# Performance work log

Measured on AMD Instinct MI355X. Metric: run time of the kernel, lower is better.

Reference implementation:

```python
import jax, jax.numpy as jnp
import numpy as np

N_CLASS = 20          # foreground classes (VOC)
SCORE_THR = 0.05
NMS_THR = 0.3
IMG_H, IMG_W = 600, 800
R = 2000              # number of proposed ROIs


def setup_inputs() -> dict:
    key = jax.random.key(0)
    k1, k2, k3, k4, k5 = jax.random.split(key, 5)
    # well-formed proposal boxes (y1, x1, y2, x2)
    cy = jax.random.uniform(k1, (R,), minval=0.0, maxval=float(IMG_H))
    cx = jax.random.uniform(k2, (R,), minval=0.0, maxval=float(IMG_W))
    hw = jax.random.uniform(k3, (R, 2), minval=20.0, maxval=200.0)
    h, w = hw[:, 0], hw[:, 1]
    boxes = jnp.stack([
        jnp.clip(cy - 0.5 * h, 0.0, IMG_H),
        jnp.clip(cx - 0.5 * w, 0.0, IMG_W),
        jnp.clip(cy + 0.5 * h, 0.0, IMG_H),
        jnp.clip(cx + 0.5 * w, 0.0, IMG_W),
    ], axis=1).astype(jnp.float32)
    loc = (0.2 * jax.random.normal(k4, (R, 4 * (N_CLASS + 1)))).astype(jnp.float32)
    score = (2.0 * jax.random.normal(k5, (R, N_CLASS + 1))).astype(jnp.float32)
    return {
        "proposed_roi_bboxes": boxes,
        "predicted_roi_loc": loc,
        "predicted_roi_score": score,
        "img_height": IMG_H,
        "img_width": IMG_W,
    }


def _pairwise_iou(b):
    # b: [N, 4] in (y1, x1, y2, x2); IoU is invariant to axis order
    tl = jnp.maximum(b[:, None, :2], b[None, :, :2])
    br = jnp.minimum(b[:, None, 2:], b[None, :, 2:])
    wh = jnp.clip(br - tl, 0.0)
    inter = wh[..., 0] * wh[..., 1]
    area = (b[:, 2] - b[:, 0]) * (b[:, 3] - b[:, 1])
    union = area[:, None] + area[None, :] - inter
    return inter / jnp.maximum(union, 1e-9)


def _nms_keep(boxes_sorted, valid_sorted, thr):
    # boxes sorted by descending score; returns keep mask [N]
    N = boxes_sorted.shape[0]
    iou = _pairwise_iou(boxes_sorted)          # [N, N]
    idx = jnp.arange(N)
    def body(suppressed, i):
        keep_i = valid_sorted[i] & (~suppressed[i])
        suppressed = suppressed | (keep_i & (iou[i] > thr) & (idx > i))
        return suppressed, keep_i
    _, keep = jax.lax.scan(body, jnp.zeros((N,), bool), idx)
    return keep


def _detect(proposed_roi_bboxes, predicted_roi_loc, predicted_roi_score, H, W):
    Rn = proposed_roi_bboxes.shape[0]
    C1 = N_CLASS + 1
    b = proposed_roi_bboxes
    loc = predicted_roi_loc.reshape(Rn, C1, 4)
    # Utility.loc2bbox (y1,x1,y2,x2 <-> cy,cx,h,w)
    src_h = b[:, 2] - b[:, 0]
    src_w = b[:, 3] - b[:, 1]
    src_cy = b[:, 0] + 0.5 * src_h
    src_cx = b[:, 1] + 0.5 * src_w
    dy, dx, dh, dw = loc[..., 0], loc[..., 1], loc[..., 2], loc[..., 3]
    cy = dy * src_h[:, None] + src_cy[:, None]
    cx = dx * src_w[:, None] + src_cx[:, None]
    hh = jnp.exp(dh) * src_h[:, None]
    ww = jnp.exp(dw) * src_w[:, None]
    boxes = jnp.stack([cy - 0.5 * hh, cx - 0.5 * ww,
                       cy + 0.5 * hh, cx + 0.5 * ww], axis=-1)  # [R, C1, 4]
    # clamp: even coords (y) to [0,H], odd coords (x) to [0,W]
    boxes = jnp.stack([
        jnp.clip(boxes[..., 0], 0.0, H),
        jnp.clip(boxes[..., 1], 0.0, W),
        jnp.clip(boxes[..., 2], 0.0, H),
        jnp.clip(boxes[..., 3], 0.0, W),
    ], axis=-1)
    prob = jax.nn.softmax(predicted_roi_score, axis=1)          # [R, C1]

    # foreground classes 1..N_CLASS -> leading class axis [C, R, ...]
    fg_boxes = jnp.transpose(boxes[:, 1:, :], (1, 0, 2))        # [C, R, 4]
    fg_prob = prob[:, 1:].T                                     # [C, R]
    valid = fg_prob > SCORE_THR
    sort_key = jnp.where(valid, fg_prob, -jnp.inf)
    order = jnp.argsort(-sort_key, axis=1)                      # [C, R]
    boxes_s = jnp.take_along_axis(fg_boxes, order[..., None], axis=1)
    prob_s = jnp.take_along_axis(fg_prob, order, axis=1)
    valid_s = jnp.take_along_axis(valid, order, axis=1)

    keep = jax.vmap(_nms_keep, in_axes=(0, 0, None))(boxes_s, valid_s, NMS_THR)  # [C, R] bool

    km = keep.astype(boxes_s.dtype)
    out = jnp.concatenate([boxes_s, prob_s[..., None]], axis=-1) * km[..., None]  # [C, R, 5]
    labels = jnp.arange(1, N_CLASS + 1, dtype=boxes_s.dtype)[:, None] * km        # [C, R]
    return out, labels, keep


def reference(proposed_roi_bboxes, predicted_roi_loc, predicted_roi_score,
              img_height, img_width):
    out, labels, keep = _detect(proposed_roi_bboxes, predicted_roi_loc,
                                predicted_roi_score, float(img_height), float(img_width))
    return out, labels, keep
```

## Files before the change

kernel.cpp:

```cpp
#include <hip/hip_runtime.h>
#include <cstdint>

#pragma clang fp contract(off)

#define R_N   2000
#define C1    21
#define NCLS  20
#define MAXFV 512
#define OUT_LBL   200000
#define OUT_KEEP  240000
#define FMARGIN   4.0f

__device__ __forceinline__ double read_dim(const void* p) {
  int iv = *(const int*)p;
  if (iv >= 1 && iv <= 1000000) return (double)iv;
  float fv = *(const float*)p;
  if (fv >= 1.0f && fv <= 1000000.0f) return (double)fv;
  return *(const double*)p;
}

__global__ __launch_bounds__(256) void prep3_kernel(
    const float* __restrict__ rois, const float* __restrict__ loc,
    const float* __restrict__ score,
    const void* __restrict__ hptr, const void* __restrict__ wptr,
    double4* __restrict__ dbox_all, double* __restrict__ prob_t)
{
  int tid = blockIdx.x * 256 + threadIdx.x;
  if (tid < 40000) {
    int r = tid % R_N, c = tid / R_N;
    const double H = read_dim(hptr), W = read_dim(wptr);
    const float* l4 = loc + r * 84 + (c + 1) * 4;
    double dy = (double)l4[0], dx = (double)l4[1];
    double eh = exp((double)l4[2]), ew = exp((double)l4[3]);
    double b0 = (double)rois[r*4+0], b1 = (double)rois[r*4+1];
    double b2 = (double)rois[r*4+2], b3 = (double)rois[r*4+3];
    double sh  = b2 - b0,       sw  = b3 - b1;
    double scy = b0 + 0.5*sh,   scx = b1 + 0.5*sw;
    double cy = dy*sh + scy,    cx = dx*sw + scx;
    double hh = eh*sh,          ww = ew*sw;
    double y1 = fmin(fmax(cy - 0.5*hh, 0.0), H);
    double x1 = fmin(fmax(cx - 0.5*ww, 0.0), W);
    double y2 = fmin(fmax(cy + 0.5*hh, 0.0), H);
    double x2 = fmin(fmax(cx + 0.5*ww, 0.0), W);
    dbox_all[c * R_N + r] = make_double4(y1, x1, y2, x2);
  } else if (tid >= 40960 && tid < 40960 + R_N) {
    int r = tid - 40960;
    const float* sc = score + r * C1;
    double m = (double)sc[0];
    #pragma unroll
    for (int k = 1; k < C1; ++k) m = fmax(m, (double)sc[k]);
    double e[C1]; double s = 0.0;
    #pragma unroll
    for (int k = 0; k < C1; ++k) { e[k] = exp((double)sc[k] - m); s += e[k]; }
    #pragma unroll
    for (int c = 0; c < NCLS; ++c) prob_t[c * R_N + r] = e[c + 1] / s;
  }
}

__global__ __launch_bounds__(256) void sortexport_kernel(
    const float* __restrict__ rois, const float* __restrict__ loc,
    const float* __restrict__ score,
    const void* __restrict__ hptr, const void* __restrict__ wptr,
    float* __restrict__ out,
    const double4* __restrict__ dbox_all, const double* __restrict__ prob_t,
    float4* __restrict__ fbox4, double4* __restrict__ dbox4s,
    float* __restrict__ farea, float* __restrict__ sprobg,
    int* __restrict__ vcls, int mode)
{
  __shared__ double sbd[R_N][4];
  __shared__ ulonglong2 keys[2048];
  __shared__ double klist64[2][64][5];
  __shared__ float  klist32[2][64][5];
  __shared__ int kcnt[2];
  __shared__ int wsum[4];

  const int cls = blockIdx.x;
  const int t = threadIdx.x;
  const int lane = t & 63, wid = t >> 6;

  ulonglong2 rk[8];
  int vmask = 0;
  #pragma unroll
  for (int u = 0; u < 8; ++u) {
    int r = t + 256 * u;
    rk[u] = make_ulonglong2(0ull, 0ull);
    if (r < R_N) {
      double p;
      if (mode) {
        p = prob_t[cls * R_N + r];
      } else {
        const float* sc = score + r * C1;
        double m = (double)sc[0];
        #pragma unroll
        for (int k = 1; k < C1; ++k) m = fmax(m, (double)sc[k]);
        double s = 0.0;
        #pragma unroll
        for (int k = 0; k < C1; ++k) s += exp((double)sc[k] - m);
        p = exp((double)sc[cls + 1] - m) / s;
      }
      if (p > 0.05) {
        rk[u] = make_ulonglong2((unsigned long long)__double_as_longlong(p),
                                (unsigned long long)(unsigned int)(~r));
        vmask |= 1 << u;
      }
    }
  }

  int cnt = __popc(vmask);
  int x = cnt;
  #pragma unroll
  for (int off = 1; off < 64; off <<= 1) {
    int y = __shfl_up(x, off);
    if (lane >= off) x += y;
  }
  if (lane == 63) wsum[wid] = x;
  __syncthreads();
  int woff = 0;
  #pragma unroll
  for (int w2 = 0; w2 < 4; ++w2) { int s = wsum[w2]; if (w2 < wid) woff += s; }
  const int V = wsum[0] + wsum[1] + wsum[2] + wsum[3];
  int pos = woff + x - cnt;
  #pragma unroll
  for (int u = 0; u < 8; ++u)
    if ((vmask >> u) & 1) keys[pos++] = rk[u];

  int NSORT = 64; while (NSORT < V) NSORT <<= 1;
  for (int j = V + t; j < NSORT; j += 256)
    keys[j] = make_ulonglong2(0ull, (unsigned long long)(unsigned int)(~(unsigned)j));
  __syncthreads();

  for (int k = 2; k <= NSORT; k <<= 1) {
    for (int js = k >> 1; js > 0; js >>= 1) {
      for (int p = t; p < (NSORT >> 1); p += 256) {
        int i = ((p & ~(js - 1)) << 1) | (p & (js - 1));
        int j = i | js;
        ulonglong2 a = keys[i], b = keys[j];
        bool altb = (a.x < b.x) || (a.x == b.x && a.y < b.y);
        if (altb == ((i & k) == 0)) { keys[i] = b; keys[j] = a; }
      }
      __syncthreads();
    }
  }

  if (mode && V <= MAXFV) {
    for (int j = t; j < V; j += 256) {
      ulonglong2 kj = keys[j];
      int idx = (int)(~(unsigned)kj.y);
      double4 bd = dbox_all[cls * R_N + idx];
      int g = cls * MAXFV + j;
      fbox4[g]  = make_float4((float)bd.x, (float)bd.y, (float)bd.z, (float)bd.w);
      dbox4s[g] = bd;
      farea[g]  = (float)((bd.z - bd.x) * (bd.w - bd.y));
      sprobg[g] = (float)__longlong_as_double((long long)kj.x);
    }
    if (t == 0) vcls[cls] = V;
    return;
  }
  if (mode && t == 0) vcls[cls] = V;

  #pragma unroll
  for (int u = 0; u < 8; ++u) {
    int r = t + 256 * u;
    if (r < R_N) {
      if (mode) {
        double4 bd = dbox_all[cls * R_N + r];
        sbd[r][0]=bd.x; sbd[r][1]=bd.y; sbd[r][2]=bd.z; sbd[r][3]=bd.w;
      } else {
        const double H = read_dim(hptr), W = read_dim(wptr);
        const float* l4 = loc + r * 84 + (cls + 1) * 4;
        double dy = (double)l4[0], dx = (double)l4[1];
        double eh = exp((double)l4[2]), ew = exp((double)l4[3]);
        double b0 = (double)rois[r*4+0], b1 = (double)rois[r*4+1];
        double b2 = (double)rois[r*4+2], b3 = (double)rois[r*4+3];
        double sh  = b2 - b0,       sw  = b3 - b1;
        double scy = b0 + 0.5*sh,   scx = b1 + 0.5*sw;
        double cy = dy*sh + scy,    cx = dx*sw + scx;
        double hh = eh*sh,          ww = ew*sw;
        sbd[r][0] = fmin(fmax(cy - 0.5*hh, 0.0), H);
        sbd[r][1] = fmin(fmax(cx - 0.5*ww, 0.0), W);
        sbd[r][2] = fmin(fmax(cy + 0.5*hh, 0.0), H);
        sbd[r][3] = fmin(fmax(cx + 0.5*ww, 0.0), W);
      }
    }
  }
  __syncthreads();

  int   idx8[8];
  float fx0[8], fx1[8], fx2[8], fx3[8], far5[8], pr[8];
  unsigned am = 0, km = 0;
  #pragma unroll
  for (int q = 0; q < 8; ++q) {
    int j = t + 256 * q;
    fx0[q]=fx1[q]=fx2[q]=fx3[q]=far5[q]=pr[q]=0.f; idx8[q]=0;
    if (j < V) {
      int idx = (int)(~(unsigned)keys[j].y);
      idx8[q] = idx;
      double a0=sbd[idx][0], a1=sbd[idx][1], a2=sbd[idx][2], a3=sbd[idx][3];
      fx0[q]=(float)a0; fx1[q]=(float)a1; fx2[q]=(float)a2; fx3[q]=(float)a3;
      far5[q]=(float)((a2-a0)*(a3-a1));
      pr[q]=(float)__longlong_as_double((long long)keys[j].x);
      am |= 1u << q;
    }
  }

  #pragma unroll
  for (int q = 0; q < 8; ++q) {
    if (256 * q >= V) break;
    for (int sub = 0; sub < 4; ++sub) {
      const int ch = 4 * q + sub;
      if (64 * ch >= V) break;
      const int buf = ch & 1;
      if (wid == sub) {
        const int s = 64 * ch + lane;
        bool a = ((am >> q) & 1u) != 0u;
        int myidx = idx8[q];
        float f0=fx0[q], f1=fx1[q], f2=fx2[q], f3=fx3[q], fa=far5[q];
        unsigned long long m = __ballot(a);
        unsigned long long kept = 0;
        while (m) {
          int i = __ffsll(m) - 1;
          m &= m - 1;
          kept |= 1ull << i;
          float k0=__shfl(f0,i), k1=__shfl(f1,i), k2=__shfl(f2,i), k3=__shfl(f3,i), ka=__shfl(fa,i);
          bool aliveL = ((m >> lane) & 1ull) != 0ull;
          float ty=fmaxf(k0,f0), tx=fmaxf(k1,f1);
          float by=fminf(k2,f2), bz=fminf(k3,f3);
          float w0=fmaxf(by-ty,0.f), w1=fmaxf(bz-tx,0.f);
          float inter=w0*w1;
          float uni=fmaxf(ka+fa-inter, 1e-9f);
          float rhs=0.3f*uni;
          bool kill = aliveL && (inter > rhs + FMARGIN);
          bool amb  = aliveL && !kill && (inter > rhs - FMARGIN);
          if (__any(amb)) {
            int kidx = __shfl(myidx, i);
            double b0=sbd[kidx][0], b1=sbd[kidx][1], b2=sbd[kidx][2], b3=sbd[kidx][3];
            double bar=(b2-b0)*(b3-b1);
            if (amb) {
              double a0=sbd[myidx][0], a1=sbd[myidx][1], a2=sbd[myidx][2], a3=sbd[myidx][3];
              double aar=(a2-a0)*(a3-a1);
              double ty_=fmax(b0,a0), tx_=fmax(b1,a1);
              double by_=fmin(b2,a2), bz_=fmin(b3,a3);
              double w0_=fmax(by_-ty_,0.0), w1_=fmax(bz_-tx_,0.0);
              double in_=w0_*w1_;
              double un_=bar+aar-in_;
              if (in_/fmax(un_,1e-9) > 0.3) kill = true;
            }
          }
          m &= ~__ballot(kill);
        }
        am &= ~(1u << q);
        if ((kept >> lane) & 1ull) {
          km |= 1u << q;
          int kpos = (int)__popcll(kept & ((1ull << lane) - 1ull));
          double a0=sbd[myidx][0], a1=sbd[myidx][1], a2=sbd[myidx][2], a3=sbd[myidx][3];
          klist64[buf][kpos][0]=a0; klist64[buf][kpos][1]=a1;
          klist64[buf][kpos][2]=a2; klist64[buf][kpos][3]=a3;
          klist64[buf][kpos][4]=(a2-a0)*(a3-a1);
          klist32[buf][kpos][0]=f0; klist32[buf][kpos][1]=f1;
          klist32[buf][kpos][2]=f2; klist32[buf][kpos][3]=f3; klist32[buf][kpos][4]=fa;
        }
        if (lane == 0) kcnt[buf] = (int)__popcll(kept);
      }
      __syncthreads();
      const int nk = kcnt[buf];
      const int jmin = 64 * (ch + 1);
      for (int n = 0; n < nk; ++n) {
        float k0=klist32[buf][n][0], k1=klist32[buf][n][1];
        float k2=klist32[buf][n][2], k3=klist32[buf][n][3], ka=klist32[buf][n][4];
        #pragma unroll
        for (int q2 = 0; q2 < 8; ++q2) {
          if (256 * q2 >= V) break;
          int j2 = t + 256 * q2;
          if (((am >> q2) & 1u) && j2 >= jmin) {
            float ty=fmaxf(k0,fx0[q2]), tx=fmaxf(k1,fx1[q2]);
            float by=fminf(k2,fx2[q2]), bz=fminf(k3,fx3[q2]);
            float w0=fmaxf(by-ty,0.f), w1=fmaxf(bz-tx,0.f);
            float inter=w0*w1;
            float uni=fmaxf(ka+far5[q2]-inter, 1e-9f);
            float rhs=0.3f*uni;
            if (inter > rhs + FMARGIN) {
              am &= ~(1u << q2);
            } else if (inter > rhs - FMARGIN) {
              int idx = idx8[q2];
              double a0=sbd[idx][0], a1=sbd[idx][1], a2=sbd[idx][2], a3=sbd[idx][3];
              double ar_=(a2-a0)*(a3-a1);
              double b0=klist64[buf][n][0], b1=klist64[buf][n][1];
              double b2=klist64[buf][n][2], b3=klist64[buf][n][3], br=klist64[buf][n][4];
              double ty_=fmax(b0,a0), tx_=fmax(b1,a1);
              double by_=fmin(b2,a2), bz_=fmin(b3,a3);
              double w0_=fmax(by_-ty_,0.0), w1_=fmax(bz_-tx_,0.0);
              double in_=w0_*w1_;
              double un_=br+ar_-in_;
              if (in_/fmax(un_,1e-9) > 0.3) am &= ~(1u << q2);
            }
          }
        }
      }
    }
  }

  #pragma unroll
  for (int u = 0; u < 8; ++u) {
    int j = t + 256 * u;
    if (j < R_N) {
      int row = cls * R_N + j;
      bool k = ((km >> u) & 1u) != 0u;
      out[row*5+0] = k ? fx0[u] : 0.f;
      out[row*5+1] = k ? fx1[u] : 0.f;
      out[row*5+2] = k ? fx2[u] : 0.f;
      out[row*5+3] = k ? fx3[u] : 0.f;
      out[row*5+4] = k ? pr[u]  : 0.f;
      out[OUT_LBL  + row] = k ? (float)(cls + 1) : 0.f;
      out[OUT_KEEP + row] = k ? 1.f : 0.f;
    }
  }
}

__global__ __launch_bounds__(256) void build_kernel(
    const float4* __restrict__ fbox4, const float* __restrict__ farea,
    const double4* __restrict__ dbox4s, const int* __restrict__ vcls,
    unsigned long long* __restrict__ kw)
{
  const int cls = blockIdx.x;
  const int V = vcls[cls];
  if (V > MAXFV) return;
  int n = blockIdx.y * 256 + threadIdx.x;
  int c = 0;
  #pragma unroll
  for (int cc = 1; cc < 8; ++cc) if (n >= 32*cc*(cc+1)) c = cc;
  int rem = n - 32*c*(c+1);
  int jq = rem / (c + 1);
  int j = 64*c + jq;
  int w = rem - jq*(c+1);
  if (j >= V) return;

  const float4* fb = fbox4 + cls * MAXFV;
  const float*  fa = farea + cls * MAXFV;
  float4 mb = fb[j];
  float  ma = fa[j];
  int i0 = 64*w;
  int i1 = min(i0 + 64, j);
  unsigned long long acc = 0ull;
  #pragma unroll 8
  for (int i = i0; i < i1; ++i) {
    float4 bb = fb[i]; float ba = fa[i];
    float ty=fmaxf(bb.x,mb.x), tx=fmaxf(bb.y,mb.y);
    float by=fminf(bb.z,mb.z), bz=fminf(bb.w,mb.w);
    float w0=fmaxf(by-ty,0.f), w1=fmaxf(bz-tx,0.f);
    float inter=w0*w1;
    float uni=fmaxf(ba+ma-inter, 1e-9f);
    float rhs=0.3f*uni;
    bool kill = inter > rhs + FMARGIN;
    if (!kill && inter > rhs - FMARGIN) {
      double4 bd = dbox4s[cls*MAXFV + i];
      double4 md = dbox4s[cls*MAXFV + j];
      double bar=(bd.z-bd.x)*(bd.w-bd.y);
      double dar=(md.z-md.x)*(md.w-md.y);
      double ty_=fmax(bd.x,md.x), tx_=fmax(bd.y,md.y);
      double by_=fmin(bd.z,md.z), bz_=fmin(bd.w,md.w);
      double w0_=fmax(by_-ty_,0.0), w1_=fmax(bz_-tx_,0.0);
      double in_=w0_*w1_;
      double un_=bar+dar-in_;
      kill = in_/fmax(un_,1e-9) > 0.3;
    }
    acc |= (unsigned long long)(kill ? 1 : 0) << (i & 63);
  }
  kw[(size_t)(cls*MAXFV + j)*8 + w] = acc;
}

__global__ __launch_bounds__(256) void scan_kernel(
    float* __restrict__ out,
    const float4* __restrict__ fbox4, const float* __restrict__ sprobg,
    const unsigned long long* __restrict__ kw, const int* __restrict__ vcls)
{
  __shared__ unsigned long long ckill[2][8][256];
  __shared__ unsigned long long keptm[8];
  const int cls = blockIdx.x;
  const int V = vcls[cls];
  if (V > MAXFV) return;
  const int t = threadIdx.x, lane = t & 63, wid = t >> 6;

  unsigned long long ckq[2] = {0ull, 0ull};
  unsigned am = 0;
  #pragma unroll
  for (int q = 0; q < 2; ++q) {
    int j = t + 256*q;
    if (j < V) {
      am |= 1u << q;
      const unsigned long long* src = kw + (size_t)(cls*MAXFV + j)*8;
      int c = wid + 4*q;
      for (int w = 0; w < c; ++w) ckill[q][w][t] = src[w];
      ckq[q] = src[c];
    }
  }

  unsigned km = 0;
  #pragma unroll
  for (int q = 0; q < 2; ++q) {
    if (256*q >= V) break;
    for (int sub = 0; sub < 4; ++sub) {
      const int ch = 4*q + sub;
      if (64*ch >= V) break;
      if (wid == sub) {
        bool a = ((am >> q) & 1u) != 0u;
        unsigned long long m = __ballot(a);
        unsigned long long kept = 0ull;
        while (m) {
          int i = __ffsll(m) - 1;
          unsigned long long bit = 1ull << i;
          kept |= bit; m &= ~bit;
          bool kill = ((ckq[q] >> i) & 1ull) != 0ull;
          m &= ~__ballot(kill);
        }
        am &= ~(1u << q);
        if ((kept >> lane) & 1ull) km |= 1u << q;
        if (lane == 0) keptm[ch] = kept;
      }
      __syncthreads();
      unsigned long long K = keptm[ch];
      #pragma unroll
      for (int q2 = 0; q2 < 2; ++q2) {
        if (256*q2 >= V) break;
        if (((am >> q2) & 1u) && (wid + 4*q2) > ch) {
          if (ckill[q2][ch][t] & K) am &= ~(1u << q2);
        }
      }
    }
  }

  #pragma unroll
  for (int u = 0; u < 8; ++u) {
    int j = t + 256*u;
    if (j < R_N) {
      int row = cls*R_N + j;
      bool k = (u < 2) && ((km >> u) & 1u);
      float v0=0.f, v1=0.f, v2=0.f, v3=0.f, v4=0.f;
      if (k) {
        float4 b = fbox4[cls*MAXFV + j];
        v0=b.x; v1=b.y; v2=b.z; v3=b.w; v4=sprobg[cls*MAXFV + j];
      }
      out[row*5+0]=v0; out[row*5+1]=v1; out[row*5+2]=v2; out[row*5+3]=v3; out[row*5+4]=v4;
      out[OUT_LBL  + row] = k ? (float)(cls + 1) : 0.f;
      out[OUT_KEEP + row] = k ? 1.f : 0.f;
    }
  }
}

extern "C" void kernel_launch(void* const* d_in, const int* in_sizes, int n_in,
                              void* d_out, int out_size, void* d_ws, size_t ws_size,
                              hipStream_t stream) {
  const float* rois  = (const float*)d_in[0];
  const float* loc   = (const float*)d_in[1];
  const float* score = (const float*)d_in[2];
  const void*  hp    = d_in[3];
  const void*  wp    = d_in[4];
  float* out = (float*)d_out;

  char* wsb = (char*)d_ws;
  double4* dbox_all = (double4*)(wsb + 0);
  double*  prob_t   = (double*)(wsb + 1280000);
  float4*  fbox4    = (float4*)(wsb + 1600000);
  double4* dbox4s   = (double4*)(wsb + 1763840);
  float*   farea    = (float*)(wsb + 2091520);
  float*   sprob    = (float*)(wsb + 2132480);
  unsigned long long* kw = (unsigned long long*)(wsb + 2173440);
  int*     vcls     = (int*)(wsb + 2828800);
  const size_t WS_NEED = 2828880;

  if (ws_size >= WS_NEED) {
    prep3_kernel<<<dim3(168), dim3(256), 0, stream>>>(rois, loc, score, hp, wp,
                                                      dbox_all, prob_t);
    sortexport_kernel<<<dim3(NCLS), dim3(256), 0, stream>>>(
        rois, loc, score, hp, wp, out, dbox_all, prob_t,
        fbox4, dbox4s, farea, sprob, vcls, 1);
    build_kernel<<<dim3(NCLS, 9), dim3(256), 0, stream>>>(fbox4, farea, dbox4s, vcls, kw);
    scan_kernel<<<dim3(NCLS), dim3(256), 0, stream>>>(out, fbox4, sprob, kw, vcls);
  } else {
    sortexport_kernel<<<dim3(NCLS), dim3(256), 0, stream>>>(
        rois, loc, score, hp, wp, out, (const double4*)nullptr, (const double*)nullptr,
        (float4*)nullptr, (double4*)nullptr, (float*)nullptr, (float*)nullptr,
        (int*)nullptr, 0);
  }
}
```

Before: 55.72 us.

## Use wave-local bitonic stages and move output zeroing into prep kernel

The bitonic sort in the sort kernel now runs the small-stride stages (js < 128) within each wavefront on a 128-element slice, synchronised with an LDS waitcnt rather than a block-wide barrier. Only the large-stride stages still use __syncthreads. Output zero-fill moves into the highly parallel prep kernel, so the scan kernel writes only kept rows instead of all 2000 rows per class. This removes many block barriers and serial per-class stores. The risks are LDS ordering correctness within a wave and a write-after-zero dependency across kernels.

```diff
diff --git a/kernel.cpp b/kernel.cpp
--- a/kernel.cpp
+++ b/kernel.cpp
@@ -11,6 +11,12 @@
 #define OUT_KEEP  240000
 #define FMARGIN   4.0f
 
+#define WAVE_SYNC() do {                                        \
+  __builtin_amdgcn_sched_barrier(0);                            \
+  asm volatile("s_waitcnt lgkmcnt(0)" ::: "memory");            \
+  __builtin_amdgcn_sched_barrier(0);                            \
+} while (0)
+
 __device__ __forceinline__ double read_dim(const void* p) {
   int iv = *(const int*)p;
   if (iv >= 1 && iv <= 1000000) return (double)iv;
@@ -23,9 +29,13 @@
     const float* __restrict__ rois, const float* __restrict__ loc,
     const float* __restrict__ score,
     const void* __restrict__ hptr, const void* __restrict__ wptr,
-    double4* __restrict__ dbox_all, double* __restrict__ prob_t)
+    double4* __restrict__ dbox_all, double* __restrict__ prob_t,
+    float* __restrict__ out)
 {
   int tid = blockIdx.x * 256 + threadIdx.x;
+  float4 z4 = make_float4(0.f, 0.f, 0.f, 0.f);
+  for (int z = tid; z < 70000; z += 168 * 256) ((float4*)out)[z] = z4;
+
   if (tid < 40000) {
     int r = tid % R_N, c = tid / R_N;
     const double H = read_dim(hptr), W = read_dim(wptr);
@@ -129,18 +139,37 @@
     keys[j] = make_ulonglong2(0ull, (unsigned long long)(unsigned int)(~(unsigned)j));
   __syncthreads();
 
+  const int wb = 128 * wid;
+  int wsz = NSORT - wb; if (wsz > 128) wsz = 128;
   for (int k = 2; k <= NSORT; k <<= 1) {
-    for (int js = k >> 1; js > 0; js >>= 1) {
-      for (int p = t; p < (NSORT >> 1); p += 256) {
-        int i = ((p & ~(js - 1)) << 1) | (p & (js - 1));
-        int j = i | js;
-        ulonglong2 a = keys[i], b = keys[j];
-        bool altb = (a.x < b.x) || (a.x == b.x && a.y < b.y);
-        if (altb == ((i & k) == 0)) { keys[i] = b; keys[j] = a; }
+    int js = k >> 1;
+    if (js >= 128) {
+      for (; js >= 128; js >>= 1) {
+        __syncthreads();
+        for (int p = t; p < (NSORT >> 1); p += 256) {
+          int i = ((p & ~(js - 1)) << 1) | (p & (js - 1));
+          int j = i | js;
+          ulonglong2 a = keys[i], b = keys[j];
+          bool altb = (a.x < b.x) || (a.x == b.x && a.y < b.y);
+          if (altb == ((i & k) == 0)) { keys[i] = b; keys[j] = a; }
+        }
       }
       __syncthreads();
     }
-  }
+    if (wsz > 0) {
+      for (; js > 0; js >>= 1) {
+        if (lane < (wsz >> 1)) {
+          int i = wb + (((lane & ~(js - 1)) << 1) | (lane & (js - 1)));
+          int j = i | js;
+          ulonglong2 a = keys[i], b = keys[j];
+          bool altb = (a.x < b.x) || (a.x == b.x && a.y < b.y);
+          if (altb == ((i & k) == 0)) { keys[i] = b; keys[j] = a; }
+        }
+        WAVE_SYNC();
+      }
+    }
+  }
+  __syncthreads();
 
   if (mode && V <= MAXFV) {
     for (int j = t; j < V; j += 256) {
@@ -429,19 +458,15 @@
   }
 
   #pragma unroll
-  for (int u = 0; u < 8; ++u) {
-    int j = t + 256*u;
-    if (j < R_N) {
+  for (int q = 0; q < 2; ++q) {
+    int j = t + 256*q;
+    if (j < V && ((km >> q) & 1u)) {
       int row = cls*R_N + j;
-      bool k = (u < 2) && ((km >> u) & 1u);
-      float v0=0.f, v1=0.f, v2=0.f, v3=0.f, v4=0.f;
-      if (k) {
-        float4 b = fbox4[cls*MAXFV + j];
-        v0=b.x; v1=b.y; v2=b.z; v3=b.w; v4=sprobg[cls*MAXFV + j];
-      }
-      out[row*5+0]=v0; out[row*5+1]=v1; out[row*5+2]=v2; out[row*5+3]=v3; out[row*5+4]=v4;
-      out[OUT_LBL  + row] = k ? (float)(cls + 1) : 0.f;
-      out[OUT_KEEP + row] = k ? 1.f : 0.f;
+      float4 b = fbox4[cls*MAXFV + j];
+      out[row*5+0]=b.x; out[row*5+1]=b.y; out[row*5+2]=b.z; out[row*5+3]=b.w;
+      out[row*5+4]=sprobg[cls*MAXFV + j];
+      out[OUT_LBL  + row] = (float)(cls + 1);
+      out[OUT_KEEP + row] = 1.f;
     }
   }
 }
@@ -469,7 +494,7 @@
 
   if (ws_size >= WS_NEED) {
     prep3_kernel<<<dim3(168), dim3(256), 0, stream>>>(rois, loc, score, hp, wp,
-                                                      dbox_all, prob_t);
+                                                      dbox_all, prob_t, out);
     sortexport_kernel<<<dim3(NCLS), dim3(256), 0, stream>>>(
         rois, loc, score, hp, wp, out, dbox_all, prob_t,
         fbox4, dbox4s, farea, sprob, vcls, 1);
```

Result: faster. 52.55 us, median of 3 (-5.7%).
